# Kernel optimization log

Measured on AMD Instinct MI355X. Metric: run time of the kernel, lower is better.

The kernel has to match this reference:

```python
import jax, jax.numpy as jnp
import numpy as np

MAX_FREQ = 10
CORR_RADIUS = 2
PATCH = 9


def _gelu(x):
    return jax.nn.gelu(x, approximate=False)


def _project(coords, R, C0, f, pp):
    # coords [N,3] -> uv [ncams,N,2], cam-space z [ncams,N]
    d = coords[None, :, :] - C0[:, None, :]
    Xc = jnp.einsum('cij,cnj->cni', R, d)
    z = jnp.maximum(Xc[..., 2:3], 1e-6)
    uv = Xc[..., :2] / z * f[:, None, :] + pp[:, None, :]
    return uv, Xc[..., 2]


def _fourier(x, max_freq):
    freqs = (2.0 ** jnp.arange(max_freq, dtype=x.dtype)) * jnp.pi
    xf = x[..., None] * freqs
    enc = jnp.concatenate([jnp.sin(xf), jnp.cos(xf)], axis=-1)  # [...,D,2F]
    return enc.reshape(enc.shape[:-2] + (x.shape[-1] * 2 * max_freq,))


def _bilinear_time(img, t, gx, gy):
    # img [B,T,C,H,W]; t [B,K] int; gx,gy [B,K,P] normalized grid in [-1,1]
    # grid_sample(align_corners=False, padding_mode='zeros') via direct 4-tap gather
    B, T, C, H, W = img.shape
    x = (gx + 1.0) * 0.5 * W - 0.5
    y = (gy + 1.0) * 0.5 * H - 0.5
    x0 = jnp.floor(x)
    y0 = jnp.floor(y)
    wx = (x - x0)[..., None]
    wy = (y - y0)[..., None]
    x0 = x0.astype(jnp.int32)
    y0 = y0.astype(jnp.int32)
    b = jnp.arange(B)[:, None, None]
    tt = t[:, :, None]

    def tap(yy, xx):
        ok = ((xx >= 0) & (xx < W) & (yy >= 0) & (yy < H))[..., None]
        v = img[b, tt, :, jnp.clip(yy, 0, H - 1), jnp.clip(xx, 0, W - 1)]  # [B,K,P,C]
        return v * ok.astype(v.dtype)

    return (tap(y0, x0) * (1 - wx) * (1 - wy) + tap(y0, x0 + 1) * wx * (1 - wy)
            + tap(y0 + 1, x0) * (1 - wx) * wy + tap(y0 + 1, x0 + 1) * wx * wy)


def _conv2d(x, w, b):
    y = jax.lax.conv_general_dilated(x, w, (1, 1), 'SAME', dimension_numbers=('NCHW', 'OIHW', 'NCHW'))
    return y + b[None, :, None, None]


def _conv3d(x, w, b):
    y = jax.lax.conv_general_dilated(x, w, (1, 1, 1), 'SAME', dimension_numbers=('NCDHW', 'OIDHW', 'NCDHW'))
    return y + b[None, :, None, None, None]


def reference(views, cam_R, cam_center, cam_focal, cam_pp, query_coords, query_time, target_time, cube_scale, v2v_w, v2v_b, lin_vol_w, lin_vol_b, lin_pos_w, lin_pos_b, lin_depth_w, lin_depth_b, conv1_w, conv1_b, conv2_w, conv2_b, conv3_w, conv3_b, mlp1_w, mlp1_b, mlp2_w, mlp2_b, tq_emb, tt_emb, vis_emb_tab, depth_norm_scale, gate_w, gate_b, fus1_w, fus1_b, fus2_w, fus2_b):
    ncams, B, T, C, H, W = views.shape
    K = query_coords.shape[1]
    sizes = jnp.asarray([W, H], dtype=query_coords.dtype)

    # project query points to all cameras
    qflat = query_coords.reshape(-1, 3)
    p2d_flat, zc = _project(qflat, cam_R, cam_center, cam_focal, cam_pp)  # [ncams,BK,2]
    p2d_full = p2d_flat.reshape(ncams, B, K, 2)

    # fourier position embedding
    pp_n = jnp.transpose(p2d_full, (1, 2, 0, 3)) / sizes  # [B,K,ncams,2]
    embed_pos = _fourier(pp_n, MAX_FREQ) @ lin_pos_w.T + lin_pos_b

    # volume embedding: masked multi-camera cube sampling + 3D conv
    cs = 2 * CORR_RADIUS + 1
    P3 = cs ** 3
    row = (jnp.arange(cs, dtype=query_coords.dtype) - CORR_RADIUS) * (cube_scale * 2.0)
    gx3, gy3, gz3 = jnp.meshgrid(row, row, row, indexing='ij')
    xyz = jnp.stack([gx3, gy3, gz3], axis=-1).reshape(-1, 3)  # [P3,3], x outermost
    cube = (query_coords[:, :, None, :] + xyz).reshape(-1, 3)
    pc, _ = _project(cube, cam_R, cam_center, cam_focal, cam_pp)
    pc = pc.reshape(ncams, B, K, P3, 2)
    smps, msks = [], []
    for c in range(ncams):
        g = 2.0 * pc[c] / sizes - 1.0
        m = (g[..., 0] >= -1) & (g[..., 0] <= 1) & (g[..., 1] >= -1) & (g[..., 1] <= 1)
        s = _bilinear_time(views[c], query_time, g[..., 0], g[..., 1])  # [B,K,P3,C]
        smps.append(s)
        msks.append(m)
    vol = jnp.stack(smps)  # [ncams,B,K,P3,C]
    mf = jnp.stack(msks).astype(vol.dtype)[..., None]
    cnt = jnp.maximum(mf.sum(0), 1.0)
    mv = (vol * mf).sum(0) / cnt  # [B,K,P3,C]
    mv = mv.reshape(B, K, cs, cs, cs, C)  # (x,y,z,C)
    mv = jnp.transpose(mv, (0, 1, 5, 4, 3, 2)).reshape(B * K, C, cs, cs, cs)  # [(BK),C,z,y,x]
    mv = _gelu(_conv3d(mv, v2v_w, v2v_b))  # EmbedV2V: Conv3d(3,vdim,3) + GELU
    vd = mv.shape[1]
    mv = mv.reshape(B, K, vd, cs, cs, cs)
    mv = jnp.transpose(mv, (0, 1, 2, 5, 4, 3)).reshape(B, K, vd * P3)  # 'b t 1 (d total)'
    embed_volume = mv @ lin_vol_w.T + lin_vol_b
    embed_volume = jnp.broadcast_to(embed_volume[:, :, None, :], (B, K, ncams, embed_volume.shape[-1]))

    # patch embedding per camera
    lin = jnp.arange(PATCH, dtype=query_coords.dtype)
    gyy, gxx = jnp.meshgrid(lin, lin, indexing='ij')
    offs = jnp.stack([gxx - (PATCH - 1) / 2.0, gyy - (PATCH - 1) / 2.0], axis=-1)  # [P,P,2]
    pats = []
    for c in range(ncams):
        px = p2d_full[c][:, :, None, None, :] + offs  # [B,K,P,P,2]
        g = ((2.0 * px + 1.0) / sizes - 1.0).reshape(B, K, PATCH * PATCH, 2)
        s = _bilinear_time(views[c], query_time, g[..., 0], g[..., 1])  # [B,K,PP,C]
        pats.append(jnp.transpose(s.reshape(B, K, PATCH, PATCH, C), (0, 1, 4, 2, 3)))
    patches = jnp.stack(pats).reshape(ncams * B * K, C, PATCH, PATCH)
    x = _gelu(_conv2d(patches, conv1_w, conv1_b))
    x = _gelu(_conv2d(x, conv2_w, conv2_b))
    x = _gelu(_conv2d(x, conv3_w, conv3_b))
    x = x.reshape(x.shape[0], -1)  # 'b c p q -> b (c p q)'
    x = _gelu(x @ mlp1_w.T + mlp1_b)  # dropout is eval-mode identity
    emb_p = x @ mlp2_w.T + mlp2_b
    embed_patch = jnp.transpose(emb_p.reshape(ncams, B, K, -1), (1, 2, 0, 3))

    E = tq_emb.shape[1]
    embed_qt = jnp.broadcast_to(tq_emb[query_time][:, :, None, :], (B, K, ncams, E))
    embed_tt = jnp.broadcast_to(tt_emb[target_time][:, :, None, :], (B, K, ncams, E))

    # visibility (pinhole in-bounds check with margin=2)
    u = p2d_flat[..., 0]
    v = p2d_flat[..., 1]
    margin = 2.0
    vis = (zc > 0) & (u >= margin) & (u <= W - margin) & (v >= margin) & (v <= H - margin)
    vis = jnp.transpose(vis.reshape(ncams, B, K), (1, 2, 0))  # [B,K,ncams]
    embed_vis = vis_emb_tab[vis.astype(jnp.int32)]

    depths = jnp.linalg.norm(query_coords[:, :, None, :] - cam_center, axis=-1) / (cube_scale * depth_norm_scale[0])
    embed_depth = _fourier(depths[..., None], MAX_FREQ) @ lin_depth_w.T + lin_depth_b

    # gated fusion of 7 terms + fusion MLP
    terms = [embed_pos, embed_volume, embed_patch, embed_qt, embed_tt, embed_vis, embed_depth]
    gates = jax.nn.sigmoid(jnp.concatenate(terms, axis=-1) @ gate_w.T + gate_b)  # [B,K,ncams,7]
    fused = sum(gates[..., i:i + 1] * terms[i] for i in range(len(terms)))
    h = _gelu(fused @ fus1_w.T + fus1_b)
    embed_total = h @ fus2_w.T + fus2_b  # [B,K,ncams,decoder_dim]
    return embed_total, vis


def setup_inputs():
    ks = jax.random.split(jax.random.key(0), 24)
    ncams, B, T, C, H, W = 4, 2, 16, 3, 256, 256
    K, E, MF, cs, P, vdim = 256, 256, 10, 5, 9, 8
    views = jax.random.normal(ks[0], (ncams, B, T, C, H, W), jnp.float32)
    cam_R = jnp.tile(jnp.eye(3, dtype=jnp.float32)[None], (ncams, 1, 1))
    cam_center = jnp.stack([jnp.linspace(-0.5, 0.5, ncams), jnp.linspace(0.5, -0.5, ncams), jnp.full((ncams,), -5.0)], axis=-1).astype(jnp.float32)
    cam_focal = jnp.full((ncams, 2), 200.0, jnp.float32)
    cam_pp = jnp.full((ncams, 2), 128.0, jnp.float32)
    query_coords = jax.random.uniform(ks[1], (B, K, 3), jnp.float32, -1.0, 1.0)
    query_time = jax.random.randint(ks[2], (B, K), 0, T).astype(jnp.int32)
    target_time = jax.random.randint(ks[3], (B, K), 0, T).astype(jnp.int32)
    cube_scale = jnp.float32(0.02)

    def w(k, shape, s=0.02):
        return jax.random.normal(k, shape, jnp.float32) * s

    z = lambda n: jnp.zeros((n,), jnp.float32)
    return dict(
        views=views, cam_R=cam_R, cam_center=cam_center, cam_focal=cam_focal, cam_pp=cam_pp,
        query_coords=query_coords, query_time=query_time, target_time=target_time, cube_scale=cube_scale,
        v2v_w=w(ks[4], (vdim, C, 3, 3, 3)), v2v_b=z(vdim),
        lin_vol_w=w(ks[5], (E, cs ** 3 * vdim)), lin_vol_b=z(E),
        lin_pos_w=w(ks[6], (E, 4 * MF)), lin_pos_b=z(E),
        lin_depth_w=w(ks[7], (E, 2 * MF)), lin_depth_b=z(E),
        conv1_w=w(ks[8], (32, 3, 3, 3)), conv1_b=z(32),
        conv2_w=w(ks[9], (64, 32, 3, 3)), conv2_b=z(64),
        conv3_w=w(ks[10], (128, 64, 3, 3)), conv3_b=z(128),
        mlp1_w=w(ks[11], (2 * E, 128 * P * P)), mlp1_b=z(2 * E),
        mlp2_w=w(ks[12], (E, 2 * E)), mlp2_b=z(E),
        tq_emb=w(ks[13], (T, E), 1.0), tt_emb=w(ks[14], (T, E), 1.0),
        vis_emb_tab=w(ks[15], (2, E), 1.0),
        depth_norm_scale=jnp.array([500.0], jnp.float32),
        gate_w=w(ks[16], (7, 7 * E), 0.01), gate_b=z(7),
        fus1_w=w(ks[17], (4 * E, E)), fus1_b=z(4 * E),
        fus2_w=w(ks[18], (E, 4 * E)), fus2_b=z(E),
    )
```

## Files before the change

### kernel.cpp

```cpp
#include <hip/hip_runtime.h>
#include <hip/hip_bf16.h>

typedef __hip_bfloat16 bf16;
typedef __attribute__((ext_vector_type(8))) short short8;
typedef __attribute__((ext_vector_type(4))) float floatx4;

#define NC 4
#define BB 2
#define TS 16
#define CHN 3
#define HH 256
#define WW 256
#define KQ 256
#define EE 256
#define BKT 512
#define HW 65536
#define NSEG 25
#define CH1 32
#define CH1P 40
#define CH2 64
#define CH2P 72
#define PW 11

#define PB_WCL   32
#define PB_W23   160
#define PB_AUXW  416
#define PB_PROJ  424
#define PB_CUBE  936
#define PB_M1W   1448
#define PB_END   1452

__device__ __forceinline__ float tof(bf16 x){ return __bfloat162float(x); }
__device__ __forceinline__ bf16 tobf(float x){ return __float2bfloat16(x); }
__device__ __forceinline__ float gelu_f(float x){
    float t = fabsf(x) * 0.70710678118654752f;
    float k = __builtin_amdgcn_rcpf(fmaf(0.3275911f, t, 1.f));
    float p = fmaf(fmaf(fmaf(fmaf(1.061405429f, k, -1.453152027f), k,
                   1.421413741f), k, -0.284496736f), k, 0.254829592f) * k;
    float e = __expf(-t*t);
    float er = fmaf(-p, e, 1.f);
    float s = copysignf(er, x);
    return 0.5f*x*(1.f + s);
}
__device__ __forceinline__ float ldx(const void* p, size_t i, int bf){
    return bf ? tof(((const bf16*)p)[i]) : ((const float*)p)[i];
}
__device__ __forceinline__ void gload_lds16(const void* g, void* l){
    __builtin_amdgcn_global_load_lds((const __attribute__((address_space(1))) void*)g,
                                     (__attribute__((address_space(3))) void*)l, 16, 0, 0);
}
__device__ __forceinline__ unsigned pack2(float a, float b){
    union{ bf16 h[2]; unsigned u; } pk; pk.h[0]=tobf(a); pk.h[1]=tobf(b); return pk.u;
}

struct CvtArgs { const void* src[NSEG]; int dstoff[NSEG]; int cnt[NSEG]; };

struct PrepArgs {
    const void *camF, *camR, *camC, *camP, *qc, *csc;
    const void *c2w, *c3w, *linv, *f1w, *f2w, *m2w, *m1w, *views;
    const void *v2vw, *v2vb;
    const void *linpw, *lindw;
    const int* qtime;
    bf16 *w2cl, *w3cl, *linv_bf, *f1w_bf, *f2w_bf, *m2w_bf, *m1w_bf;
    float *p2d, *visf;
    float *linpwT, *lindwT;
    bf16* volf;
    void* dout;
    int* flagp;
};

union PrepSm {
    struct { float vol[3][7][7][7]; float ws[648]; float bs[8]; } cube;
    bf16 lin[10368];
};

__global__ __launch_bounds__(256) void prep_kernel(CvtArgs ca, float* __restrict__ pool, PrepArgs a)
{
    int bid = blockIdx.x, tid = threadIdx.x;
    int bf = (((const unsigned short*)a.camF)[0] != 0) ? 1 : 0;
    __shared__ PrepSm sm;

    if (bid < PB_WCL){
        for (int s=0; s<NSEG; ++s){
            const void* src = ca.src[s];
            float* d = pool + ca.dstoff[s];
            int n = ca.cnt[s];
            for (int i = bid*256 + tid; i < n; i += PB_WCL*256) d[i] = ldx(src, i, bf);
        }
    } else if (bid < PB_W23){
        int i0 = (bid-PB_WCL)*256 + tid;
        const int stride = (PB_W23-PB_WCL)*256;
        for (int i=i0; i<64*32*9; i+=stride){
            int oc=i/(32*9), r=i%(32*9), ic=r/9, tap=r%9;
            a.w2cl[tap*(64*CH1) + oc*CH1 + ic] = tobf(ldx(a.c2w, i, bf));
        }
        for (int i=i0; i<128*64*9; i+=stride){
            int oc=i/(64*9), r=i%(64*9), ic=r/9, tap=r%9;
            a.w3cl[tap*(128*CH2) + oc*CH2 + ic] = tobf(ldx(a.c3w, i, bf));
        }
    } else if (bid < PB_AUXW){
        int sub = (bid-PB_W23)>>6;
        int i0 = ((bid-PB_W23)&63)*256 + tid;
        const int stride = 64*256;
        if (sub==0){
            for (int i=i0; i<256*1024; i+=stride){
                int r=i>>10, c=i&1023;
                a.linv_bf[i] = tobf(c<1000 ? ldx(a.linv, (size_t)r*1000+c, bf) : 0.f);
            }
        } else if (sub==1){
            for (int i=i0; i<1024*256; i+=stride) a.f1w_bf[i]=tobf(ldx(a.f1w,i,bf));
        } else if (sub==2){
            for (int i=i0; i<256*1024; i+=stride) a.f2w_bf[i]=tobf(ldx(a.f2w,i,bf));
        } else {
            for (int i=i0; i<256*512; i+=stride) a.m2w_bf[i]=tobf(ldx(a.m2w,i,bf));
        }
    } else if (bid < PB_PROJ){
        if (bid==PB_AUXW && tid==0) *a.flagp = bf;
        int idx = (bid-PB_AUXW)*256 + tid;
        if (idx < NC*BKT){
            int c = idx / BKT, bk = idx % BKT;
            float dx = ldx(a.qc,bk*3+0,bf) - ldx(a.camC,c*3+0,bf);
            float dy = ldx(a.qc,bk*3+1,bf) - ldx(a.camC,c*3+1,bf);
            float dz = ldx(a.qc,bk*3+2,bf) - ldx(a.camC,c*3+2,bf);
            float X0 = ldx(a.camR,c*9+0,bf)*dx + ldx(a.camR,c*9+1,bf)*dy + ldx(a.camR,c*9+2,bf)*dz;
            float X1 = ldx(a.camR,c*9+3,bf)*dx + ldx(a.camR,c*9+4,bf)*dy + ldx(a.camR,c*9+5,bf)*dz;
            float X2 = ldx(a.camR,c*9+6,bf)*dx + ldx(a.camR,c*9+7,bf)*dy + ldx(a.camR,c*9+8,bf)*dz;
            float z = fmaxf(X2, 1e-6f);
            float u = X0/z*ldx(a.camF,c*2+0,bf) + ldx(a.camP,c*2+0,bf);
            float v = X1/z*ldx(a.camF,c*2+1,bf) + ldx(a.camP,c*2+1,bf);
            a.p2d[idx*2+0] = u; a.p2d[idx*2+1] = v;
            bool vis = (X2 > 0.f) && (u >= 2.f) && (u <= (float)WW-2.f) && (v >= 2.f) && (v <= (float)HH-2.f);
            a.visf[idx] = vis ? 1.f : 0.f;
            float vv = vis ? 1.f : 0.f;
            size_t vidx = (size_t)BB*KQ*NC*EE + (size_t)bk*NC + c;
            if (bf) ((bf16*)a.dout)[vidx] = tobf(vv);
            else    ((float*)a.dout)[vidx] = vv;
        }
    } else if (bid < PB_CUBE){
        int bk = bid - PB_PROJ;
        int c = tid & 3;
        int pg = tid >> 2;
        int b = bk >> 8;
        for (int i=tid; i<3*343; i+=256) ((float*)sm.cube.vol)[i]=0.f;
        for (int i=tid; i<648; i+=256) sm.cube.ws[i]=ldx(a.v2vw,i,bf);
        if (tid<8) sm.cube.bs[tid]=ldx(a.v2vb,tid,bf);
        __syncthreads();
        float cs2 = ldx(a.csc,0,bf) * 2.f;
        int t = a.qtime[bk];
        float qx0 = ldx(a.qc,bk*3+0,bf);
        float qy0 = ldx(a.qc,bk*3+1,bf);
        float qz0 = ldx(a.qc,bk*3+2,bf);
        float R0=ldx(a.camR,c*9+0,bf), R1=ldx(a.camR,c*9+1,bf), R2=ldx(a.camR,c*9+2,bf);
        float R3=ldx(a.camR,c*9+3,bf), R4=ldx(a.camR,c*9+4,bf), R5=ldx(a.camR,c*9+5,bf);
        float R6=ldx(a.camR,c*9+6,bf), R7=ldx(a.camR,c*9+7,bf), R8=ldx(a.camR,c*9+8,bf);
        float Cx=ldx(a.camC,c*3+0,bf), Cy=ldx(a.camC,c*3+1,bf), Cz=ldx(a.camC,c*3+2,bf);
        float Fx=ldx(a.camF,c*2+0,bf), Fy=ldx(a.camF,c*2+1,bf);
        float Px=ldx(a.camP,c*2+0,bf), Py=ldx(a.camP,c*2+1,bf);
        #pragma unroll
        for (int pass=0; pass<2; ++pass){
            int p = (pass<<6) + pg;
            bool act = p < 125;
            int i=p/25, j=(p/5)%5, kz=p%5;
            float a0=0.f,a1=0.f,a2=0.f,ms=0.f;
            if (act){
                float qx = qx0 + (float)(i-2)*cs2;
                float qy = qy0 + (float)(j-2)*cs2;
                float qz = qz0 + (float)(kz-2)*cs2;
                float dx=qx-Cx, dy=qy-Cy, dz=qz-Cz;
                float X0=R0*dx+R1*dy+R2*dz;
                float X1=R3*dx+R4*dy+R5*dz;
                float X2=R6*dx+R7*dy+R8*dz;
                float z = fmaxf(X2,1e-6f);
                float u = X0/z*Fx+Px, v = X1/z*Fy+Py;
                if (u>=0.f && u<=(float)WW && v>=0.f && v<=(float)HH){
                    ms = 1.f;
                    float x = u-0.5f, y = v-0.5f;
                    float xf = floorf(x), yf = floorf(y);
                    int ix=(int)xf, iy=(int)yf;
                    float wx=x-xf, wy=y-yf;
                    size_t basev = (size_t)((c*BB+b)*TS + t)*CHN*HW;
                    float wxs[2]={1.f-wx,wx}, wys[2]={1.f-wy,wy};
                    #pragma unroll
                    for (int ty=0;ty<2;++ty){
                        int yy=iy+ty; if (yy<0||yy>=HH) continue;
                        #pragma unroll
                        for (int tx=0;tx<2;++tx){
                            int xx=ix+tx; if (xx<0||xx>=WW) continue;
                            float wt=wys[ty]*wxs[tx];
                            size_t o = basev + (size_t)yy*WW+xx;
                            a0 += wt*ldx(a.views,o,bf);
                            a1 += wt*ldx(a.views,o+HW,bf);
                            a2 += wt*ldx(a.views,o+2*HW,bf);
                        }
                    }
                }
            }
            a0 += __shfl_xor(a0,1); a0 += __shfl_xor(a0,2);
            a1 += __shfl_xor(a1,1); a1 += __shfl_xor(a1,2);
            a2 += __shfl_xor(a2,1); a2 += __shfl_xor(a2,2);
            ms += __shfl_xor(ms,1); ms += __shfl_xor(ms,2);
            if (act && c==0){
                float cnt = fmaxf(ms,1.f);
                sm.cube.vol[0][kz+1][j+1][i+1]=a0/cnt;
                sm.cube.vol[1][kz+1][j+1][i+1]=a1/cnt;
                sm.cube.vol[2][kz+1][j+1][i+1]=a2/cnt;
            }
        }
        __syncthreads();
        if (tid >= 104 && tid < 128) a.volf[bk*1024 + 1000 + (tid-104)] = tobf(0.f);
        if (tid < 125){
            int w2=tid/25, h2=(tid/5)%5, d2=tid%5;
            for (int oc=0;oc<8;++oc){
                float acc = sm.cube.bs[oc];
                #pragma unroll
                for (int ic=0;ic<3;++ic)
                  #pragma unroll
                  for (int dz=0;dz<3;++dz)
                    #pragma unroll
                    for (int dy=0;dy<3;++dy)
                      #pragma unroll
                      for (int dxx=0;dxx<3;++dxx)
                        acc += sm.cube.vol[ic][d2+dz][h2+dy][w2+dxx] * sm.cube.ws[(((oc*3+ic)*3+dz)*3+dy)*3+dxx];
                a.volf[bk*1024 + oc*125 + tid] = tobf(gelu_f(acc));
            }
        }
    } else if (bid < PB_M1W){
        int n = bid - PB_CUBE;
        const size_t off = (size_t)n*10368;
        if (bf){
            const bf16* s = (const bf16*)a.m1w + off;
            for (int i=tid;i<10368;i+=256) sm.lin[i]=s[i];
        } else {
            const float* s = (const float*)a.m1w + off;
            for (int i=tid;i<10368;i+=256) sm.lin[i]=tobf(s[i]);
        }
        __syncthreads();
        unsigned* d = (unsigned*)(a.m1w_bf + off);
        for (int j2=tid; j2<5184; j2+=256){
            int j = j2*2;
            int pos0=j>>7, oc0=j&127;
            int pos1=(j+1)>>7, oc1=(j+1)&127;
            d[j2] = pack2(tof(sm.lin[oc0*81+pos0]), tof(sm.lin[oc1*81+pos1]));
        }
    } else {
        int i0 = (bid-PB_M1W)*256 + tid;
        for (int o=i0; o<10240; o+=1024){
            int j=o>>8, e=o&255;
            a.linpwT[o] = ldx(a.linpw, (size_t)e*40+j, bf);
        }
        for (int o=i0; o<5120; o+=1024){
            int j=o>>8, e=o&255;
            a.lindwT[o] = ldx(a.lindw, (size_t)e*20+j, bf);
        }
    }
}

struct __align__(16) PCShared {
    union __align__(16) {
        bf16 a2cl[11*PW*CH2P];
        struct { float w1s[864]; float patch[3][11][11]; } c1;
    } u;
    __align__(16) bf16 a1cl[11*PW*CH1P];
};
struct __align__(16) LVShared {
    bf16 As[64][72];
    bf16 Bs[64][72];
};
struct __align__(16) G128Shared {
    bf16 As[128][64];
    bf16 Bs[128][64];
};

__device__ __forceinline__ void patchconv_body(
    PCShared& sm, int img,
    const void* __restrict__ views, const float* __restrict__ p2d,
    const int* __restrict__ qtime,
// ... 176 lines not shown
        #pragma unroll
        for (int kk=0; kk<64; kk+=32){
            short8 af = *(const short8*)&sm.As[arow][kk+koff];
            #pragma unroll
            for (int j=0;j<4;++j){
                short8 wf = *(const short8*)&sm.Bs[(j<<4)+nrow][kk+koff];
                acc[j] = __builtin_amdgcn_mfma_f32_16x16x32_bf16(af, wf, acc[j], 0,0,0);
            }
        }
        __syncthreads();
    }
    float* out = lvparts + (size_t)z * (512*256);
    int crow = (wave<<4) + ((lane>>4)<<2);
    int ccol = lane&15;
    #pragma unroll
    for (int j=0;j<4;++j){
        int n = n0 + (j<<4) + ccol;
        #pragma unroll
        for (int rr=0;rr<4;++rr)
            out[(size_t)(m0+crow+rr)*256 + n] = acc[j][rr];
    }
}

__global__ __launch_bounds__(256) void patchlin_kernel(
    const void* __restrict__ views, const float* __restrict__ p2d,
    const int* __restrict__ qtime,
    const float* __restrict__ w1, const float* __restrict__ b1,
    const bf16* __restrict__ w2cl, const float* __restrict__ b2,
    const bf16* __restrict__ w3cl, const float* __restrict__ b3,
    bf16* __restrict__ act_out, int img0, int npc, const int* __restrict__ flagp,
    const bf16* __restrict__ volf, const bf16* __restrict__ linvw,
    float* __restrict__ lvparts)
{
    __shared__ union { PCShared pc; LVShared lv; } sm;
    int bid = blockIdx.x;
    if (bid < npc){
        patchconv_body(sm.pc, img0+bid, views, p2d, qtime, w1, b1, w2cl, b2, w3cl, b3,
                       act_out, flagp);
    } else {
        linvol_body(sm.lv, bid-npc, volf, linvw, lvparts);
    }
}

__global__ __launch_bounds__(256) void patchconv_kernel(
    const void* __restrict__ views, const float* __restrict__ p2d,
    const int* __restrict__ qtime,
    const float* __restrict__ w1, const float* __restrict__ b1,
    const bf16* __restrict__ w2cl, const float* __restrict__ b2,
    const bf16* __restrict__ w3cl, const float* __restrict__ b3,
    bf16* __restrict__ act_out, int img0, const int* __restrict__ flagp)
{
    __shared__ PCShared sm;
    patchconv_body(sm, img0+blockIdx.x, views, p2d, qtime, w1, b1, w2cl, b2, w3cl, b3,
                   act_out, flagp);
}

template<int OUT>
__global__ __launch_bounds__(256) void gemm_bf16_kernel(
    const bf16* __restrict__ A, const bf16* __restrict__ W, const float* __restrict__ bias,
    float* __restrict__ Cf, void* __restrict__ Cb, int M, int N, int K, int iters,
    int pstride)
{
    __shared__ bf16 As[2][64][72];
    __shared__ bf16 Bs[2][64][72];
    int tid = threadIdx.x;
    int wave = tid>>6, lane = tid&63;
    int m0 = blockIdx.y<<6, n0 = blockIdx.x<<6;
    int kt0 = blockIdx.z*iters;
    int lr = tid>>3;
    int lc = (tid&7)<<3;
    const bf16* Ap0 = A + (size_t)(m0+lr)*K    + (kt0<<6) + lc;
    const bf16* Ap1 = A + (size_t)(m0+lr+32)*K + (kt0<<6) + lc;
    const bf16* Wp0 = W + (size_t)(n0+lr)*K    + (kt0<<6) + lc;
    const bf16* Wp1 = W + (size_t)(n0+lr+32)*K + (kt0<<6) + lc;
    uint4 ra0 = *(const uint4*)Ap0;
    uint4 ra1 = *(const uint4*)Ap1;
    uint4 rb0 = *(const uint4*)Wp0;
// ... 32 lines not shown
            int nxt = cur^1;
            *(uint4*)&As[nxt][lr][lc]    = ra0;
            *(uint4*)&As[nxt][lr+32][lc] = ra1;
            *(uint4*)&Bs[nxt][lr][lc]    = rb0;
            *(uint4*)&Bs[nxt][lr+32][lc] = rb1;
            __syncthreads();
        }
    }
    int crow = (wave<<4) + ((lane>>4)<<2);
    int ccol = lane&15;
    #pragma unroll
    for (int j=0;j<4;++j){
        int n = n0 + (j<<4) + ccol;
        if (OUT==1){
            float bb = bias[n];
            #pragma unroll
            for (int r=0;r<4;++r)
                ((bf16*)Cb)[(size_t)(m0+crow+r)*N + n] = tobf(gelu_f(acc[j][r] + bb));
        } else {
            float* out = Cf + (size_t)blockIdx.z * pstride;
            #pragma unroll
            for (int r=0;r<4;++r)
                out[(size_t)(m0+crow+r)*N + n] = acc[j][r];
        }
    }
}

__global__ __launch_bounds__(256) void gemm128_kernel(
    const bf16* __restrict__ A, const bf16* __restrict__ W,
    float* __restrict__ Cf, int N, int K, int kiters_total, int zdiv, int pstride)
{
    __shared__ G128Shared s;
    int tid = threadIdx.x;
    int wave = tid>>6, lane = tid&63;
    int m0 = blockIdx.y<<7, n0 = blockIdx.x<<7;
    int it0 = (int)(((long)blockIdx.z     * kiters_total) / zdiv);
    int it1 = (int)(((long)(blockIdx.z+1) * kiters_total) / zdiv);
    float* out = Cf + (size_t)blockIdx.z * pstride;
    int srow = (wave<<5) + (lane>>3);
    int scol = (lane&7)<<3;
    const bf16* Ap = A + (size_t)(m0+srow)*K + ((size_t)it0<<6) + scol;
    const bf16* Bp = W + (size_t)(n0+srow)*K + ((size_t)it0<<6) + scol;
    bf16* AsW = &s.As[wave<<5][0];
    bf16* BsW = &s.Bs[wave<<5][0];
    floatx4 acc[4][4];
    #pragma unroll
    for (int i=0;i<4;++i)
      #pragma unroll
      for (int j=0;j<4;++j) acc[i][j] = (floatx4){0.f,0.f,0.f,0.f};
    int wm = (wave>>1)<<6, wn = (wave&1)<<6;
    int frow = lane&15, koff = (lane>>4)<<3;
    for (int it=it0; it<it1; ++it){
        size_t off = (size_t)(it-it0)<<6;
        #pragma unroll
        for (int j=0;j<4;++j){
            gload_lds16(Ap + (size_t)(j<<3)*K + off, AsW + (j<<3)*64);
            gload_lds16(Bp + (size_t)(j<<3)*K + off, BsW + (j<<3)*64);
        }
        __syncthreads();
        #pragma unroll
        for (int kk=0;kk<64;kk+=32){
            short8 af[4], bfv[4];
            #pragma unroll
            for (int i=0;i<4;++i) af[i]  = *(const short8*)&s.As[wm + (i<<4) + frow][kk+koff];
            #pragma unroll
            for (int j=0;j<4;++j) bfv[j] = *(const short8*)&s.Bs[wn + (j<<4) + frow][kk+koff];
            #pragma unroll
            for (int i=0;i<4;++i)
              #pragma unroll
              for (int j=0;j<4;++j)
                acc[i][j] = __builtin_amdgcn_mfma_f32_16x16x32_bf16(af[i], bfv[j], acc[i][j], 0,0,0);
        }
        __syncthreads();
    }
    int crow = (lane>>4)<<2;
    int ccol = lane&15;
    #pragma unroll
    for (int i=0;i<4;++i){
        int mrow = m0 + wm + (i<<4) + crow;
        #pragma unroll
        for (int j=0;j<4;++j){
            int n = n0 + wn + (j<<4) + ccol;
            #pragma unroll
            for (int r=0;r<4;++r)
                out[(size_t)(mrow+r)*N + n] = acc[i][j][r];
        }
    }
}

__global__ __launch_bounds__(256) void mlp1_fin_kernel(const float* __restrict__ P,
                                                       const float* __restrict__ bias,
                                                       bf16* __restrict__ Cb, int total, int Nmask,
                                                       int pstride){
    for (int i = blockIdx.x*256 + threadIdx.x; i < total; i += gridDim.x*256){
        float s = bias[i & Nmask];
        #pragma unroll
        for (int p=0;p<8;++p) s += P[(size_t)p*pstride + i];
        Cb[i] = tobf(gelu_f(s));
    }
}

__global__ __launch_bounds__(256) void fin2_kernel(const float* __restrict__ P,
                                                   const float* __restrict__ bias,
                                                   void* __restrict__ out, const int* __restrict__ flagp,
                                                   int total, int mask, int pstride){
    int bf = *flagp;
    for (int i = blockIdx.x*256 + threadIdx.x; i < total; i += gridDim.x*256){
        float s = bias[i & mask];
// ... 154 lines not shown
    int NCH = (ws_size >= 103353856ull) ? 1 : 2;
    int MCH = 2048 / NCH;
    bf16*  c3act    = (bf16*)(base + 27332096);
    bf16*  hbuf_bf  = (bf16*)(base + 27332096);
    float* m2parts  = (float*)(base + 31526400);
    float* f2parts  = (float*)(base + 35720704);
    float* parts    = (float*)(base + 27332096 + (size_t)MCH*10368*2);

    PrepArgs pa;
    pa.camF=d_in[3]; pa.camR=d_in[1]; pa.camC=d_in[2]; pa.camP=d_in[4];
    pa.qc=d_in[5]; pa.csc=d_in[8];
    pa.c2w=d_in[19]; pa.c3w=d_in[21];
    pa.linv=d_in[11]; pa.f1w=d_in[33]; pa.f2w=d_in[35]; pa.m2w=d_in[25];
    pa.m1w=d_in[23]; pa.views=views;
    pa.v2vw=d_in[9]; pa.v2vb=d_in[10];
    pa.linpw=d_in[13]; pa.lindw=d_in[15];
    pa.qtime=qtime;
    pa.w2cl=w2cl; pa.w3cl=w3cl; pa.linv_bf=linv_bf; pa.f1w_bf=f1w_bf;
    pa.f2w_bf=f2w_bf; pa.m2w_bf=m2w_bf; pa.m1w_bf=m1w_bf;
    pa.p2d=p2d; pa.visf=visf; pa.volf=volf_bf;
    pa.linpwT=linpwT; pa.lindwT=lindwT;
    pa.dout=d_out; pa.flagp=flag;

    prep_kernel<<<PB_END, 256, 0, stream>>>(ca, pool, pa);

    if (NCH == 1){
        patchlin_kernel<<<2048+256, 256, 0, stream>>>(views, p2d, qtime, P_c1w, P_c1b,
                                                      w2cl, P_c2b, w3cl, P_c3b, c3act, 0, 2048, flag,
                                                      volf_bf, linv_bf, lvparts);
        gemm128_kernel<<<dim3(4, 16, 8), 256, 0, stream>>>(c3act, m1w_bf, parts,
                                                           512, 10368, 162, 8, 2048*512);
        mlp1_fin_kernel<<<512, 256, 0, stream>>>(parts, P_m1b, mlp1o_bf, 2048*512, 511, 2048*512);
    } else {
        gemm_bf16_kernel<2><<<dim3(4,8,8), 256, 0, stream>>>(volf_bf, linv_bf, nullptr, lvparts, nullptr,
                                                             512, 256, 1024, 2, 512*256);
        for (int ch=0; ch<NCH; ++ch){
            int img0 = ch*MCH;
            patchconv_kernel<<<MCH, 256, 0, stream>>>(views, p2d, qtime, P_c1w, P_c1b,
                                                      w2cl, P_c2b, w3cl, P_c3b, c3act, img0, flag);
            gemm128_kernel<<<dim3(4, MCH/128, 8), 256, 0, stream>>>(c3act, m1w_bf, parts,
                                                                    512, 10368, 162, 8, MCH*512);
            mlp1_fin_kernel<<<512, 256, 0, stream>>>(parts, P_m1b, mlp1o_bf + (size_t)img0*512,
                                                     MCH*512, 511, MCH*512);
        }
    }
    gemm_bf16_kernel<2><<<dim3(4,32,2), 256, 0, stream>>>(mlp1o_bf, m2w_bf, nullptr, m2parts, nullptr,
                                                          2048, 256, 512, 4, 2048*256);
    terms_kernel<<<2048, 256, 0, stream>>>(p2d, visf, lvparts, P_linvb, m2parts, P_m2b,
                                           linpwT, P_linpb, lindwT, P_lindb,
                                           P_tq, P_tt, P_vtab, P_gw, P_gb,
                                           qtime, ttime, P_qc, P_camC, P_csc, P_dns, fusedb_bf);
    gemm_bf16_kernel<1><<<dim3(16,32,1), 256, 0, stream>>>(fusedb_bf, f1w_bf, P_f1b, nullptr, hbuf_bf,
                                                           2048, 1024, 256, 4, 0);
    gemm_bf16_kernel<2><<<dim3(4,32,4), 256, 0, stream>>>(hbuf_bf, f2w_bf, nullptr, f2parts, nullptr,
                                                          2048, 256, 1024, 4, 2048*256);
    fin2_kernel<<<512, 256, 0, stream>>>(f2parts, P_f2b, d_out, flag, 2048*256, 255, 2048*256);
// ... 3 lines not shown
```

Measured before the change: 376.2 us.

## Rebalance prep work across kernels to overlap with patch conv and GEMM

Splits the prep kernel so that only small conversions and the projection run first. The cube sampling/conv3d, mlp1 weight transpose and aux weight conversions now run as extra blocks inside the patch-conv launch, and the lin_vol GEMM runs alongside the mlp1 GEMM in a combined launch. This removes the serial prep phase and fills idle CUs during the patch conv and GEMM stages. The cost is a heavier mixed-role kernel whose shared-memory union is sized for its largest role, which may lower occupancy.

```diff
diff --git a/kernel.cpp b/kernel.cpp
--- a/kernel.cpp
+++ b/kernel.cpp
@@ -22,13 +22,14 @@
 #define CH2P 72
 #define PW 11
 
-#define PB_WCL   32
-#define PB_W23   160
-#define PB_AUXW  416
-#define PB_PROJ  424
-#define PB_CUBE  936
-#define PB_M1W   1448
-#define PB_END   1452
+#define Q_WCL   32
+#define Q_W23   160
+#define Q_LINV  224
+#define Q_PROJ  232
+#define Q_LPW   236
+#define Q_CUBE  748
+#define Q_M1W   1260
+#define Q_END   1452
 
 __device__ __forceinline__ float tof(bf16 x){ return __bfloat162float(x); }
 __device__ __forceinline__ bf16 tobf(float x){ return __float2bfloat16(x); }
@@ -69,10 +70,132 @@
     int* flagp;
 };
 
-union PrepSm {
-    struct { float vol[3][7][7][7]; float ws[648]; float bs[8]; } cube;
-    bf16 lin[10368];
-};
+struct CubeSM { float vol[3][7][7][7]; float ws[648]; float bs[8]; };
+
+__device__ __forceinline__ void cube_body(CubeSM& sm, int bk, int tid,
+                                          const PrepArgs& a, int bf){
+    int c = tid & 3;
+    int pg = tid >> 2;
+    int b = bk >> 8;
+    for (int i=tid; i<3*343; i+=256) ((float*)sm.vol)[i]=0.f;
+    for (int i=tid; i<648; i+=256) sm.ws[i]=ldx(a.v2vw,i,bf);
+    if (tid<8) sm.bs[tid]=ldx(a.v2vb,tid,bf);
+    __syncthreads();
+    float cs2 = ldx(a.csc,0,bf) * 2.f;
+    int t = a.qtime[bk];
+    float qx0 = ldx(a.qc,bk*3+0,bf);
+    float qy0 = ldx(a.qc,bk*3+1,bf);
+    float qz0 = ldx(a.qc,bk*3+2,bf);
+    float R0=ldx(a.camR,c*9+0,bf), R1=ldx(a.camR,c*9+1,bf), R2=ldx(a.camR,c*9+2,bf);
+    float R3=ldx(a.camR,c*9+3,bf), R4=ldx(a.camR,c*9+4,bf), R5=ldx(a.camR,c*9+5,bf);
+    float R6=ldx(a.camR,c*9+6,bf), R7=ldx(a.camR,c*9+7,bf), R8=ldx(a.camR,c*9+8,bf);
+    float Cx=ldx(a.camC,c*3+0,bf), Cy=ldx(a.camC,c*3+1,bf), Cz=ldx(a.camC,c*3+2,bf);
+    float Fx=ldx(a.camF,c*2+0,bf), Fy=ldx(a.camF,c*2+1,bf);
+    float Px=ldx(a.camP,c*2+0,bf), Py=ldx(a.camP,c*2+1,bf);
+    #pragma unroll
+    for (int pass=0; pass<2; ++pass){
+        int p = (pass<<6) + pg;
+        bool act = p < 125;
+        int i=p/25, j=(p/5)%5, kz=p%5;
+        float a0=0.f,a1=0.f,a2=0.f,ms=0.f;
+        if (act){
+            float qx = qx0 + (float)(i-2)*cs2;
+            float qy = qy0 + (float)(j-2)*cs2;
+            float qz = qz0 + (float)(kz-2)*cs2;
+            float dx=qx-Cx, dy=qy-Cy, dz=qz-Cz;
+            float X0=R0*dx+R1*dy+R2*dz;
+            float X1=R3*dx+R4*dy+R5*dz;
+            float X2=R6*dx+R7*dy+R8*dz;
+            float z = fmaxf(X2,1e-6f);
+            float u = X0/z*Fx+Px, v = X1/z*Fy+Py;
+            if (u>=0.f && u<=(float)WW && v>=0.f && v<=(float)HH){
+                ms = 1.f;
+                float x = u-0.5f, y = v-0.5f;
+                float xf = floorf(x), yf = floorf(y);
+                int ix=(int)xf, iy=(int)yf;
+                float wx=x-xf, wy=y-yf;
+                size_t basev = (size_t)((c*BB+b)*TS + t)*CHN*HW;
+                float wxs[2]={1.f-wx,wx}, wys[2]={1.f-wy,wy};
+                #pragma unroll
+                for (int ty=0;ty<2;++ty){
+                    int yy=iy+ty; if (yy<0||yy>=HH) continue;
+                    #pragma unroll
+                    for (int tx=0;tx<2;++tx){
+                        int xx=ix+tx; if (xx<0||xx>=WW) continue;
+                        float wt=wys[ty]*wxs[tx];
+                        size_t o = basev + (size_t)yy*WW+xx;
+                        a0 += wt*ldx(a.views,o,bf);
+                        a1 += wt*ldx(a.views,o+HW,bf);
+                        a2 += wt*ldx(a.views,o+2*HW,bf);
+                    }
+                }
+            }
+        }
+        a0 += __shfl_xor(a0,1); a0 += __shfl_xor(a0,2);
+        a1 += __shfl_xor(a1,1); a1 += __shfl_xor(a1,2);
+        a2 += __shfl_xor(a2,1); a2 += __shfl_xor(a2,2);
+        ms += __shfl_xor(ms,1); ms += __shfl_xor(ms,2);
+        if (act && c==0){
+            float cnt = fmaxf(ms,1.f);
+            sm.vol[0][kz+1][j+1][i+1]=a0/cnt;
+            sm.vol[1][kz+1][j+1][i+1]=a1/cnt;
+            sm.vol[2][kz+1][j+1][i+1]=a2/cnt;
+        }
+    }
+    __syncthreads();
+    if (tid >= 104 && tid < 128) a.volf[bk*1024 + 1000 + (tid-104)] = tobf(0.f);
+    if (tid < 125){
+        int w2=tid/25, h2=(tid/5)%5, d2=tid%5;
+        for (int oc=0;oc<8;++oc){
+            float acc = sm.bs[oc];
+            #pragma unroll
+            for (int ic=0;ic<3;++ic)
+              #pragma unroll
+              for (int dz=0;dz<3;++dz)
+                #pragma unroll
+                for (int dy=0;dy<3;++dy)
+                  #pragma unroll
+                  for (int dxx=0;dxx<3;++dxx)
+                    acc += sm.vol[ic][d2+dz][h2+dy][w2+dxx] * sm.ws[(((oc*3+ic)*3+dz)*3+dy)*3+dxx];
+            a.volf[bk*1024 + oc*125 + tid] = tobf(gelu_f(acc));
+        }
+    }
+}
+
+__device__ __forceinline__ void m1w_body(bf16* lin, int n, int tid,
+                                         const PrepArgs& a, int bf){
+    const size_t off = (size_t)n*10368;
+    if (bf){
+        const bf16* s = (const bf16*)a.m1w + off;
+        for (int i=tid;i<10368;i+=256) lin[i]=s[i];
+    } else {
+        const float* s = (const float*)a.m1w + off;
+        for (int i=tid;i<10368;i+=256) lin[i]=tobf(s[i]);
+    }
+    __syncthreads();
+    unsigned* d = (unsigned*)(a.m1w_bf + off);
+    for (int j2=tid; j2<5184; j2+=256){
+        int j = j2*2;
+        int pos0=j>>7, oc0=j&127;
+        int pos1=(j+1)>>7, oc1=(j+1)&127;
+        d[j2] = pack2(tof(lin[oc0*81+pos0]), tof(lin[oc1*81+pos1]));
+    }
+}
+
+__device__ __forceinline__ void aux3_body(int blk, int tid, const PrepArgs& a, int bf){
+    int sub = blk>>6;
+    int i0 = (blk&63)*256 + tid;
+    const int stride = 64*256;
+    if (sub==0){
+        for (int i=i0; i<1024*256; i+=stride) a.f1w_bf[i]=tobf(ldx(a.f1w,i,bf));
+    } else if (sub==1){
+        for (int i=i0; i<256*1024; i+=stride) a.f2w_bf[i]=tobf(ldx(a.f2w,i,bf));
+    } else {
+        for (int i=i0; i<256*512; i+=stride) a.m2w_bf[i]=tobf(ldx(a.m2w,i,bf));
+    }
+}
+
+union PrepSm { CubeSM cube; bf16 lin[10368]; };
 
 __global__ __launch_bounds__(256) void prep_kernel(CvtArgs ca, float* __restrict__ pool, PrepArgs a)
 {
@@ -80,16 +203,16 @@
     int bf = (((const unsigned short*)a.camF)[0] != 0) ? 1 : 0;
     __shared__ PrepSm sm;
 
-    if (bid < PB_WCL){
+    if (bid < Q_WCL){
         for (int s=0; s<NSEG; ++s){
             const void* src = ca.src[s];
             float* d = pool + ca.dstoff[s];
             int n = ca.cnt[s];
-            for (int i = bid*256 + tid; i < n; i += PB_WCL*256) d[i] = ldx(src, i, bf);
-        }
-    } else if (bid < PB_W23){
-        int i0 = (bid-PB_WCL)*256 + tid;
-        const int stride = (PB_W23-PB_WCL)*256;
+            for (int i = bid*256 + tid; i < n; i += Q_WCL*256) d[i] = ldx(src, i, bf);
+        }
+    } else if (bid < Q_W23){
+        int i0 = (bid-Q_WCL)*256 + tid;
+        const int stride = (Q_W23-Q_WCL)*256;
         for (int i=i0; i<64*32*9; i+=stride){
             int oc=i/(32*9), r=i%(32*9), ic=r/9, tap=r%9;
             a.w2cl[tap*(64*CH1) + oc*CH1 + ic] = tobf(ldx(a.c2w, i, bf));
@@ -98,25 +221,16 @@
             int oc=i/(64*9), r=i%(64*9), ic=r/9, tap=r%9;
             a.w3cl[tap*(128*CH2) + oc*CH2 + ic] = tobf(ldx(a.c3w, i, bf));
         }
-    } else if (bid < PB_AUXW){
-        int sub = (bid-PB_W23)>>6;
-        int i0 = ((bid-PB_W23)&63)*256 + tid;
-        const int stride = 64*256;
-        if (sub==0){
-            for (int i=i0; i<256*1024; i+=stride){
-                int r=i>>10, c=i&1023;
-                a.linv_bf[i] = tobf(c<1000 ? ldx(a.linv, (size_t)r*1000+c, bf) : 0.f);
-            }
-        } else if (sub==1){
-            for (int i=i0; i<1024*256; i+=stride) a.f1w_bf[i]=tobf(ldx(a.f1w,i,bf));
-        } else if (sub==2){
-            for (int i=i0; i<256*1024; i+=stride) a.f2w_bf[i]=tobf(ldx(a.f2w,i,bf));
-        } else {
-            for (int i=i0; i<256*512; i+=stride) a.m2w_bf[i]=tobf(ldx(a.m2w,i,bf));
-        }
-    } else if (bid < PB_PROJ){
-        if (bid==PB_AUXW && tid==0) *a.flagp = bf;
-        int idx = (bid-PB_AUXW)*256 + tid;
+    } else if (bid < Q_LINV){
+        int i0 = (bid-Q_W23)*256 + tid;
+        const int stride = (Q_LINV-Q_W23)*256;
+        for (int i=i0; i<256*1024; i+=stride){
+            int r=i>>10, c=i&1023;
+            a.linv_bf[i] = tobf(c<1000 ? ldx(a.linv, (size_t)r*1000+c, bf) : 0.f);
+        }
+    } else if (bid < Q_PROJ){
+        if (bid==Q_LINV && tid==0) *a.flagp = bf;
+        int idx = (bid-Q_LINV)*256 + tid;
         if (idx < NC*BKT){
             int c = idx / BKT, bk = idx % BKT;
             float dx = ldx(a.qc,bk*3+0,bf) - ldx(a.camC,c*3+0,bf);
@@ -136,114 +250,8 @@
             if (bf) ((bf16*)a.dout)[vidx] = tobf(vv);
             else    ((float*)a.dout)[vidx] = vv;
         }
-    } else if (bid < PB_CUBE){
-        int bk = bid - PB_PROJ;
-        int c = tid & 3;
-        int pg = tid >> 2;
-        int b = bk >> 8;
-        for (int i=tid; i<3*343; i+=256) ((float*)sm.cube.vol)[i]=0.f;
-        for (int i=tid; i<648; i+=256) sm.cube.ws[i]=ldx(a.v2vw,i,bf);
-        if (tid<8) sm.cube.bs[tid]=ldx(a.v2vb,tid,bf);
-        __syncthreads();
-        float cs2 = ldx(a.csc,0,bf) * 2.f;
-        int t = a.qtime[bk];
-        float qx0 = ldx(a.qc,bk*3+0,bf);
-        float qy0 = ldx(a.qc,bk*3+1,bf);
-        float qz0 = ldx(a.qc,bk*3+2,bf);
-        float R0=ldx(a.camR,c*9+0,bf), R1=ldx(a.camR,c*9+1,bf), R2=ldx(a.camR,c*9+2,bf);
-        float R3=ldx(a.camR,c*9+3,bf), R4=ldx(a.camR,c*9+4,bf), R5=ldx(a.camR,c*9+5,bf);
-        float R6=ldx(a.camR,c*9+6,bf), R7=ldx(a.camR,c*9+7,bf), R8=ldx(a.camR,c*9+8,bf);
-        float Cx=ldx(a.camC,c*3+0,bf), Cy=ldx(a.camC,c*3+1,bf), Cz=ldx(a.camC,c*3+2,bf);
-        float Fx=ldx(a.camF,c*2+0,bf), Fy=ldx(a.camF,c*2+1,bf);
-        float Px=ldx(a.camP,c*2+0,bf), Py=ldx(a.camP,c*2+1,bf);
-        #pragma unroll
-        for (int pass=0; pass<2; ++pass){
-            int p = (pass<<6) + pg;
-            bool act = p < 125;
-            int i=p/25, j=(p/5)%5, kz=p%5;
-            float a0=0.f,a1=0.f,a2=0.f,ms=0.f;
-            if (act){
-                float qx = qx0 + (float)(i-2)*cs2;
-                float qy = qy0 + (float)(j-2)*cs2;
-                float qz = qz0 + (float)(kz-2)*cs2;
-                float dx=qx-Cx, dy=qy-Cy, dz=qz-Cz;
-                float X0=R0*dx+R1*dy+R2*dz;
-                float X1=R3*dx+R4*dy+R5*dz;
-                float X2=R6*dx+R7*dy+R8*dz;
-                float z = fmaxf(X2,1e-6f);
-                float u = X0/z*Fx+Px, v = X1/z*Fy+Py;
-                if (u>=0.f && u<=(float)WW && v>=0.f && v<=(float)HH){
-                    ms = 1.f;
-                    float x = u-0.5f, y = v-0.5f;
-                    float xf = floorf(x), yf = floorf(y);
-                    int ix=(int)xf, iy=(int)yf;
-                    float wx=x-xf, wy=y-yf;
-                    size_t basev = (size_t)((c*BB+b)*TS + t)*CHN*HW;
-                    float wxs[2]={1.f-wx,wx}, wys[2]={1.f-wy,wy};
-                    #pragma unroll
-                    for (int ty=0;ty<2;++ty){
-                        int yy=iy+ty; if (yy<0||yy>=HH) continue;
-                        #pragma unroll
-                        for (int tx=0;tx<2;++tx){
-                            int xx=ix+tx; if (xx<0||xx>=WW) continue;
-                            float wt=wys[ty]*wxs[tx];
-                            size_t o = basev + (size_t)yy*WW+xx;
-                            a0 += wt*ldx(a.views,o,bf);
-                            a1 += wt*ldx(a.views,o+HW,bf);
-                            a2 += wt*ldx(a.views,o+2*HW,bf);
-                        }
-                    }
-                }
-            }
-            a0 += __shfl_xor(a0,1); a0 += __shfl_xor(a0,2);
-            a1 += __shfl_xor(a1,1); a1 += __shfl_xor(a1,2);
-            a2 += __shfl_xor(a2,1); a2 += __shfl_xor(a2,2);
-            ms += __shfl_xor(ms,1); ms += __shfl_xor(ms,2);
-            if (act && c==0){
-                float cnt = fmaxf(ms,1.f);
-                sm.cube.vol[0][kz+1][j+1][i+1]=a0/cnt;
-                sm.cube.vol[1][kz+1][j+1][i+1]=a1/cnt;
-                sm.cube.vol[2][kz+1][j+1][i+1]=a2/cnt;
-            }
-        }
-        __syncthreads();
-        if (tid >= 104 && tid < 128) a.volf[bk*1024 + 1000 + (tid-104)] = tobf(0.f);
-        if (tid < 125){
-            int w2=tid/25, h2=(tid/5)%5, d2=tid%5;
-            for (int oc=0;oc<8;++oc){
-                float acc = sm.cube.bs[oc];
-                #pragma unroll
-                for (int ic=0;ic<3;++ic)
-                  #pragma unroll
-                  for (int dz=0;dz<3;++dz)
-                    #pragma unroll
-                    for (int dy=0;dy<3;++dy)
-                      #pragma unroll
-                      for (int dxx=0;dxx<3;++dxx)
-                        acc += sm.cube.vol[ic][d2+dz][h2+dy][w2+dxx] * sm.cube.ws[(((oc*3+ic)*3+dz)*3+dy)*3+dxx];
-                a.volf[bk*1024 + oc*125 + tid] = tobf(gelu_f(acc));
-            }
-        }
-    } else if (bid < PB_M1W){
-        int n = bid - PB_CUBE;
-        const size_t off = (size_t)n*10368;
-        if (bf){
-            const bf16* s = (const bf16*)a.m1w + off;
-            for (int i=tid;i<10368;i+=256) sm.lin[i]=s[i];
-        } else {
-            const float* s = (const float*)a.m1w + off;
-            for (int i=tid;i<10368;i+=256) sm.lin[i]=tobf(s[i]);
-        }
-        __syncthreads();
-        unsigned* d = (unsigned*)(a.m1w_bf + off);
-        for (int j2=tid; j2<5184; j2+=256){
-            int j = j2*2;
-            int pos0=j>>7, oc0=j&127;
-            int pos1=(j+1)>>7, oc1=(j+1)&127;
-            d[j2] = pack2(tof(sm.lin[oc0*81+pos0]), tof(sm.lin[oc1*81+pos1]));
-        }
-    } else {
-        int i0 = (bid-PB_M1W)*256 + tid;
+    } else if (bid < Q_LPW){
+        int i0 = (bid-Q_PROJ)*256 + tid;
         for (int o=i0; o<10240; o+=1024){
             int j=o>>8, e=o&255;
             a.linpwT[o] = ldx(a.linpw, (size_t)e*40+j, bf);
@@ -252,6 +260,12 @@
             int j=o>>8, e=o&255;
             a.lindwT[o] = ldx(a.lindw, (size_t)e*20+j, bf);
         }
+    } else if (bid < Q_CUBE){
+        cube_body(sm.cube, bid-Q_LPW, tid, a, bf);
+    } else if (bid < Q_M1W){
+        m1w_body(sm.lin, bid-Q_CUBE, tid, a, bf);
+    } else {
+        aux3_body(bid-Q_M1W, tid, a, bf);
     }
 }
 
@@ -474,23 +488,103 @@
     }
 }
 
+__device__ __forceinline__ void gemm128_body(
+    G128Shared& s, int bid3, const bf16* __restrict__ A, const bf16* __restrict__ W,
+    float* __restrict__ Cf, int pstride)
+{
+    const int N=512, K=10368, kit=162, zdiv=8;
+    int tid = threadIdx.x;
+    int wave = tid>>6, lane = tid&63;
+    int m0 = ((bid3>>2)&15)<<7, n0 = (bid3&3)<<7;
+    int bz = bid3>>6;
+    int it0 = (int)(((long)bz     * kit) / zdiv);
+    int it1 = (int)(((long)(bz+1) * kit) / zdiv);
+    float* out = Cf + (size_t)bz * pstride;
+    int srow = (wave<<5) + (lane>>3);
+    int scol = (lane&7)<<3;
+    const bf16* Ap = A + (size_t)(m0+srow)*K + ((size_t)it0<<6) + scol;
+    const bf16* Bp = W + (size_t)(n0+srow)*K + ((size_t)it0<<6) + scol;
+    bf16* AsW = &s.As[wave<<5][0];
+    bf16* BsW = &s.Bs[wave<<5][0];
+    floatx4 acc[4][4];
+    #pragma unroll
+    for (int i=0;i<4;++i)
+      #pragma unroll
+      for (int j=0;j<4;++j) acc[i][j] = (floatx4){0.f,0.f,0.f,0.f};
+    int wm = (wave>>1)<<6, wn = (wave&1)<<6;
+    int frow = lane&15, koff = (lane>>4)<<3;
+    for (int it=it0; it<it1; ++it){
+        size_t off = (size_t)(it-it0)<<6;
+        #pragma unroll
+        for (int j=0;j<4;++j){
+            gload_lds16(Ap + (size_t)(j<<3)*K + off, AsW + (j<<3)*64);
+            gload_lds16(Bp + (size_t)(j<<3)*K + off, BsW + (j<<3)*64);
+        }
+        __syncthreads();
+        #pragma unroll
+        for (int kk=0;kk<64;kk+=32){
+            short8 af[4], bfv[4];
+            #pragma unroll
+            for (int i=0;i<4;++i) af[i]  = *(const short8*)&s.As[wm + (i<<4) + frow][kk+koff];
+            #pragma unroll
+            for (int j=0;j<4;++j) bfv[j] = *(const short8*)&s.Bs[wn + (j<<4) + frow][kk+koff];
+            #pragma unroll
+            for (int i=0;i<4;++i)
+              #pragma unroll
+              for (int j=0;j<4;++j)
+                acc[i][j] = __builtin_amdgcn_mfma_f32_16x16x32_bf16(af[i], bfv[j], acc[i][j], 0,0,0);
+        }
+        __syncthreads();
+    }
+    int crow = (lane>>4)<<2;
+    int ccol = lane&15;
+    #pragma unroll
+    for (int i=0;i<4;++i){
+        int mrow = m0 + wm + (i<<4) + crow;
+        #pragma unroll
+        for (int j=0;j<4;++j){
+            int n = n0 + wn + (j<<4) + ccol;
+            #pragma unroll
+            for (int r=0;r<4;++r)
+                out[(size_t)(mrow+r)*N + n] = acc[i][j][r];
+        }
+    }
+}
+
 __global__ __launch_bounds__(256) void patchlin_kernel(
-    const void* __restrict__ views, const float* __restrict__ p2d,
-    const int* __restrict__ qtime,
-    const float* __restrict__ w1, const float* __restrict__ b1,
-    const bf16* __restrict__ w2cl, const float* __restrict__ b2,
-    const bf16* __restrict__ w3cl, const float* __restrict__ b3,
-    bf16* __restrict__ act_out, int img0, int npc, const int* __restrict__ flagp,
+    PrepArgs a, const float* __restrict__ w1, const float* __restrict__ b1,
+    const float* __restrict__ b2, const float* __restrict__ b3,
+    bf16* __restrict__ act_out)
+{
+    __shared__ union { PCShared pc; CubeSM cube; bf16 lin[10368]; } sm;
+    int bid = blockIdx.x, tid = threadIdx.x;
+    if (bid < 2048){
+        patchconv_body(sm.pc, bid, a.views, a.p2d, a.qtime, w1, b1, a.w2cl, b2, a.w3cl, b3,
+                       act_out, a.flagp);
+    } else if (bid < 2560){
+        int bf = (((const unsigned short*)a.camF)[0] != 0) ? 1 : 0;
+        cube_body(sm.cube, bid-2048, tid, a, bf);
+    } else if (bid < 3072){
+        int bf = (((const unsigned short*)a.camF)[0] != 0) ? 1 : 0;
+        m1w_body(sm.lin, bid-2560, tid, a, bf);
+    } else {
+        int bf = (((const unsigned short*)a.camF)[0] != 0) ? 1 : 0;
+        aux3_body(bid-3072, tid, a, bf);
+    }
+}
+
+__global__ __launch_bounds__(256) void g128lv_kernel(
+    const bf16* __restrict__ A, const bf16* __restrict__ m1w_bf,
+    float* __restrict__ parts,
     const bf16* __restrict__ volf, const bf16* __restrict__ linvw,
     float* __restrict__ lvparts)
 {
-    __shared__ union { PCShared pc; LVShared lv; } sm;
+    __shared__ union { G128Shared g; LVShared lv; } sm;
     int bid = blockIdx.x;
-    if (bid < npc){
-        patchconv_body(sm.pc, img0+bid, views, p2d, qtime, w1, b1, w2cl, b2, w3cl, b3,
-                       act_out, flagp);
+    if (bid < 512){
+        gemm128_body(sm.g, bid, A, m1w_bf, parts, 2048*512);
     } else {
-        linvol_body(sm.lv, bid-npc, volf, linvw, lvparts);
+        linvol_body(sm.lv, bid-512, volf, linvw, lvparts);
     }
 }
 
@@ -505,6 +599,68 @@
     __shared__ PCShared sm;
     patchconv_body(sm, img0+blockIdx.x, views, p2d, qtime, w1, b1, w2cl, b2, w3cl, b3,
                    act_out, flagp);
+}
+
+__global__ __launch_bounds__(256) void gemm128_kernel(
+    const bf16* __restrict__ A, const bf16* __restrict__ W,
+    float* __restrict__ Cf, int N, int K, int kiters_total, int zdiv, int pstride)
+{
+    __shared__ G128Shared s;
+    int tid = threadIdx.x;
+    int wave = tid>>6, lane = tid&63;
+    int m0 = blockIdx.y<<7, n0 = blockIdx.x<<7;
+    int it0 = (int)(((long)blockIdx.z     * kiters_total) / zdiv);
+    int it1 = (int)(((long)(blockIdx.z+1) * kiters_total) / zdiv);
+    float* out = Cf + (size_t)blockIdx.z * pstride;
+    int srow = (wave<<5) + (lane>>3);
+    int scol = (lane&7)<<3;
+    const bf16* Ap = A + (size_t)(m0+srow)*K + ((size_t)it0<<6) + scol;
+    const bf16* Bp = W + (size_t)(n0+srow)*K + ((size_t)it0<<6) + scol;
+    bf16* AsW = &s.As[wave<<5][0];
+    bf16* BsW = &s.Bs[wave<<5][0];
+    floatx4 acc[4][4];
+    #pragma unroll
+    for (int i=0;i<4;++i)
+      #pragma unroll
+      for (int j=0;j<4;++j) acc[i][j] = (floatx4){0.f,0.f,0.f,0.f};
+    int wm = (wave>>1)<<6, wn = (wave&1)<<6;
+    int frow = lane&15, koff = (lane>>4)<<3;
+    for (int it=it0; it<it1; ++it){
+        size_t off = (size_t)(it-it0)<<6;
+        #pragma unroll
+        for (int j=0;j<4;++j){
+            gload_lds16(Ap + (size_t)(j<<3)*K + off, AsW + (j<<3)*64);
+            gload_lds16(Bp + (size_t)(j<<3)*K + off, BsW + (j<<3)*64);
+        }
+        __syncthreads();
+        #pragma unroll
+        for (int kk=0;kk<64;kk+=32){
+            short8 af[4], bfv[4];
+            #pragma unroll
+            for (int i=0;i<4;++i) af[i]  = *(const short8*)&s.As[wm + (i<<4) + frow][kk+koff];
+            #pragma unroll
+            for (int j=0;j<4;++j) bfv[j] = *(const short8*)&s.Bs[wn + (j<<4) + frow][kk+koff];
+            #pragma unroll
+            for (int i=0;i<4;++i)
+              #pragma unroll
+              for (int j=0;j<4;++j)
+                acc[i][j] = __builtin_amdgcn_mfma_f32_16x16x32_bf16(af[i], bfv[j], acc[i][j], 0,0,0);
+        }
+        __syncthreads();
+    }
+    int crow = (lane>>4)<<2;
+    int ccol = lane&15;
+    #pragma unroll
+    for (int i=0;i<4;++i){
+        int mrow = m0 + wm + (i<<4) + crow;
+        #pragma unroll
+        for (int j=0;j<4;++j){
+            int n = n0 + wn + (j<<4) + ccol;
+            #pragma unroll
+            for (int r=0;r<4;++r)
+                out[(size_t)(mrow+r)*N + n] = acc[i][j][r];
+        }
+    }
 }
 
 template<int OUT>
@@ -583,68 +739,6 @@
             #pragma unroll
             for (int r=0;r<4;++r)
                 out[(size_t)(m0+crow+r)*N + n] = acc[j][r];
-        }
-    }
-}
-
-__global__ __launch_bounds__(256) void gemm128_kernel(
-    const bf16* __restrict__ A, const bf16* __restrict__ W,
-    float* __restrict__ Cf, int N, int K, int kiters_total, int zdiv, int pstride)
-{
-    __shared__ G128Shared s;
-    int tid = threadIdx.x;
-    int wave = tid>>6, lane = tid&63;
-    int m0 = blockIdx.y<<7, n0 = blockIdx.x<<7;
-    int it0 = (int)(((long)blockIdx.z     * kiters_total) / zdiv);
-    int it1 = (int)(((long)(blockIdx.z+1) * kiters_total) / zdiv);
-    float* out = Cf + (size_t)blockIdx.z * pstride;
-    int srow = (wave<<5) + (lane>>3);
-    int scol = (lane&7)<<3;
-    const bf16* Ap = A + (size_t)(m0+srow)*K + ((size_t)it0<<6) + scol;
-    const bf16* Bp = W + (size_t)(n0+srow)*K + ((size_t)it0<<6) + scol;
-    bf16* AsW = &s.As[wave<<5][0];
-    bf16* BsW = &s.Bs[wave<<5][0];
-    floatx4 acc[4][4];
-    #pragma unroll
-    for (int i=0;i<4;++i)
-      #pragma unroll
-      for (int j=0;j<4;++j) acc[i][j] = (floatx4){0.f,0.f,0.f,0.f};
-    int wm = (wave>>1)<<6, wn = (wave&1)<<6;
-    int frow = lane&15, koff = (lane>>4)<<3;
-    for (int it=it0; it<it1; ++it){
-        size_t off = (size_t)(it-it0)<<6;
-        #pragma unroll
-        for (int j=0;j<4;++j){
-            gload_lds16(Ap + (size_t)(j<<3)*K + off, AsW + (j<<3)*64);
-            gload_lds16(Bp + (size_t)(j<<3)*K + off, BsW + (j<<3)*64);
-        }
-        __syncthreads();
-        #pragma unroll
-        for (int kk=0;kk<64;kk+=32){
-            short8 af[4], bfv[4];
-            #pragma unroll
-            for (int i=0;i<4;++i) af[i]  = *(const short8*)&s.As[wm + (i<<4) + frow][kk+koff];
-            #pragma unroll
-            for (int j=0;j<4;++j) bfv[j] = *(const short8*)&s.Bs[wn + (j<<4) + frow][kk+koff];
-            #pragma unroll
-            for (int i=0;i<4;++i)
-              #pragma unroll
-              for (int j=0;j<4;++j)
-                acc[i][j] = __builtin_amdgcn_mfma_f32_16x16x32_bf16(af[i], bfv[j], acc[i][j], 0,0,0);
-        }
-        __syncthreads();
-    }
-    int crow = (lane>>4)<<2;
-    int ccol = lane&15;
-    #pragma unroll
-    for (int i=0;i<4;++i){
-        int mrow = m0 + wm + (i<<4) + crow;
-        #pragma unroll
-        for (int j=0;j<4;++j){
-            int n = n0 + wn + (j<<4) + ccol;
-            #pragma unroll
-            for (int r=0;r<4;++r)
-                out[(size_t)(mrow+r)*N + n] = acc[i][j][r];
         }
     }
 }
@@ -845,16 +939,13 @@
     pa.linpwT=linpwT; pa.lindwT=lindwT;
     pa.dout=d_out; pa.flagp=flag;
 
-    prep_kernel<<<PB_END, 256, 0, stream>>>(ca, pool, pa);
-
     if (NCH == 1){
-        patchlin_kernel<<<2048+256, 256, 0, stream>>>(views, p2d, qtime, P_c1w, P_c1b,
-                                                      w2cl, P_c2b, w3cl, P_c3b, c3act, 0, 2048, flag,
-                                                      volf_bf, linv_bf, lvparts);
-        gemm128_kernel<<<dim3(4, 16, 8), 256, 0, stream>>>(c3act, m1w_bf, parts,
-                                                           512, 10368, 162, 8, 2048*512);
+        prep_kernel<<<Q_LPW, 256, 0, stream>>>(ca, pool, pa);
+        patchlin_kernel<<<3264, 256, 0, stream>>>(pa, P_c1w, P_c1b, P_c2b, P_c3b, c3act);
+        g128lv_kernel<<<768, 256, 0, stream>>>(c3act, m1w_bf, parts, volf_bf, linv_bf, lvparts);
         mlp1_fin_kernel<<<512, 256, 0, stream>>>(parts, P_m1b, mlp1o_bf, 2048*512, 511, 2048*512);
     } else {
+        prep_kernel<<<Q_END, 256, 0, stream>>>(ca, pool, pa);
         gemm_bf16_kernel<2><<<dim3(4,8,8), 256, 0, stream>>>(volf_bf, linv_bf, nullptr, lvparts, nullptr,
                                                              512, 256, 1024, 2, 512*256);
         for (int ch=0; ch<NCH; ++ch){
```

After: 390.1 us. 1.04x slower.
